# Performance work log

Measured on AMD Instinct MI355X. Metric: run time of the kernel, lower is better.

## Reference

```python
import jax, jax.numpy as jnp
import numpy as np

N = 1024       # nodes
D1 = 64        # hidden_dim_1
D2 = 64        # hidden_dim_2
E = 16384      # edges
P = 8192       # query pairs
MAXX = 100     # max node label -> Embedding(MAXX+1, D1)
EPS = 1e-5     # LayerNorm eps (no affine)


def _ln(t):
    m = jnp.mean(t, axis=-1, keepdims=True)
    v = jnp.mean((t - m) ** 2, axis=-1, keepdims=True)
    return (t - m) / jnp.sqrt(v + EPS)


def setup_inputs() -> dict:
    key = jax.random.key(0)
    ks = jax.random.split(key, 12)
    s = 0.1
    x = jax.random.randint(ks[0], (N,), 0, MAXX + 1)
    ei = jax.random.randint(ks[1], (2, E), 0, N)
    pos = jax.random.randint(ks[2], (P, 2), 0, N)
    emb = jax.random.normal(ks[3], (MAXX + 1, D1)) * s
    sage_Wl = jax.random.normal(ks[4], (2, D1, D1)) * s   # lin_l weight (aggr path, has bias)
    sage_bl = jnp.zeros((2, D1))
    sage_Wr = jax.random.normal(ks[5], (2, D1, D1)) * s   # lin_r weight (root path, no bias)
    h_W = jax.random.normal(ks[6], (D1 + 1, D2)) * s
    h_b = jnp.zeros((D2,))
    g_W = jax.random.normal(ks[7], (D1 + 1 + 2 * D2, D2)) * s
    g_b = jnp.zeros((D2,))
    lin_W = jax.random.normal(ks[8], (D2, 1)) * s
    lin_b = jnp.zeros((1,))
    return {"x": x, "ei": ei, "pos": pos, "emb": emb,
            "sage_Wl": sage_Wl, "sage_bl": sage_bl, "sage_Wr": sage_Wr,
            "h_W": h_W, "h_b": h_b, "g_W": g_W, "g_b": g_b,
            "lin_W": lin_W, "lin_b": lin_b}


def reference(x, ei, pos, emb, sage_Wl, sage_bl, sage_Wr, h_W, h_b, g_W, g_b, lin_W, lin_b):
    n = N
    src, dst = ei[0], ei[1]
    h = emb[x]                                            # (n, D1)
    # SAGEConv x2: mean-aggregate src->dst, lin_l(aggr)+bias + lin_r(root); then LN (no affine, no relu)
    deg = jax.ops.segment_sum(jnp.ones((E,), h.dtype), dst, num_segments=n)
    deg = jnp.maximum(deg, 1.0)[:, None]
    for i in range(2):
        aggr = jax.ops.segment_sum(h[src], dst, num_segments=n) / deg
        h = _ln(aggr @ sage_Wl[i] + sage_bl[i] + h @ sage_Wr[i])
    # pairwise outer product features: (n, n, D1)
    A = h[:, None, :] * h[None, :, :]
    eim = jnp.zeros((n * n,), h.dtype).at[src * n + dst].set(1.0).reshape(n, n, 1)
    A = jnp.concatenate([A, eim], axis=-1)                # (n, n, D1+1)
    # mataggr: B = h_1(A); row/col sums; D = cat(A, vec_p, vec_q); g_1(D)
    B = jax.nn.relu(_ln(A @ h_W + h_b))                   # (n, n, D2)
    vec_p = jnp.sum(B, axis=1, keepdims=True)             # (n, 1, D2)
    vec_q = jnp.sum(B, axis=0, keepdims=True)             # (1, n, D2)
    Dm = jnp.concatenate([A,
                          jnp.broadcast_to(vec_p, (n, n, D2)),
                          jnp.broadcast_to(vec_q, (n, n, D2))], axis=-1)
    G = jax.nn.relu(_ln(Dm @ g_W + g_b))                  # (n, n, D2)
    # symmetrize and gather query pairs
    S = (G * jnp.transpose(G, (1, 0, 2))).reshape(n * n, D2)
    sel = S[pos[:, 0] * n + pos[:, 1]]                    # (P, D2)
    return sel @ lin_W + lin_b                            # (P, 1)
```

## Files before the change

kernel.cpp:

```cpp
#include <hip/hip_runtime.h>
#include <hip/hip_bf16.h>

#define NN 1024
#define DD 64
#define EE 16384
#define PP 8192
#define EPSF 1e-5f
#define SWP (DD + 8)

typedef __hip_bfloat16 bf16;
typedef __attribute__((ext_vector_type(8))) short short8;
typedef __attribute__((ext_vector_type(4))) float f32x4;

static __device__ __forceinline__ float dec1(const void* src, int i, int fl) {
    if (fl) return ((const float*)src)[i];
    return __bfloat162float(((const bf16*)src)[i]);
}
static __device__ __forceinline__ unsigned short f2bf_u(float f) {
    bf16 h = __float2bfloat16(f);
    return *reinterpret_cast<unsigned short*>(&h);
}
static __device__ __forceinline__ float bfu2f(unsigned short u) {
    return __uint_as_float(((unsigned int)u) << 16);
}
static __device__ __forceinline__ int probe_fl(const void* emb) {
    int lane = threadIdx.x & 63;
    unsigned short raw = ((const unsigned short*)emb)[lane];
    float v = __uint_as_float(((unsigned int)raw) << 16);
    return (__ballot(!(fabsf(v) <= 1e3f)) != 0ull) ? 1 : 0;
}

__global__ __launch_bounds__(256) void k_prep(
        const void* __restrict__ emb, const void* __restrict__ sWl,
        const void* __restrict__ sbl, const void* __restrict__ sWr,
        const void* __restrict__ hW, const void* __restrict__ hb,
        const void* __restrict__ gW, const void* __restrict__ gb,
        const void* __restrict__ lW, const void* __restrict__ lb,
        const int* __restrict__ x, const int* __restrict__ ei,
        float* __restrict__ Wlf, float* __restrict__ blf, float* __restrict__ Wrf,
        float* __restrict__ WfT, float* __restrict__ hbw,
        float* __restrict__ gWf, float* __restrict__ linf,
        float* __restrict__ h0,
        unsigned int* __restrict__ eim, unsigned int* __restrict__ eimT,
        int* __restrict__ rowptr, int* __restrict__ csrc) {
    __shared__ int sdeg[NN];
    __shared__ int stmp[256];
    const int b = blockIdx.x, tid = threadIdx.x;
    const int fl = probe_fl(emb);

    if (b < 256) {
        int z = b * 256 + tid;
        if (z < 32768) eim[z] = 0u;
        else           eimT[z - 32768] = 0u;
    }

    if (b < 32) { int i = b * 256 + tid; Wlf[i] = dec1(sWl, i, fl); }
    else if (b == 32) { if (tid < 128) blf[tid] = dec1(sbl, tid, fl); }
    else if (b < 65) { int i = (b - 33) * 256 + tid; Wrf[i] = dec1(sWr, i, fl); }
    else if (b < 82) {
        int i = (b - 65) * 256 + tid;
        if (i < 4096) { int n = i >> 6, k = i & 63; WfT[n * DD + k] = dec1(hW, k * DD + n, fl); }
        else if (i < 4160) hbw[i - 4096] = dec1(hb, i - 4096, fl);
        else if (i < 4224) hbw[64 + (i - 4160)] = dec1(hW, 64 * DD + (i - 4160), fl);
    } else if (b < 131) {
        int i = (b - 82) * 256 + tid;
        if (i < 193 * DD) gWf[i] = dec1(gW, i, fl);
        else if (i < 194 * DD) gWf[i] = dec1(gb, i - 193 * DD, fl);
    } else if (b == 131) {
        if (tid < DD) linf[tid] = dec1(lW, tid, fl);
        else if (tid == DD) linf[DD] = dec1(lb, 0, fl);
    } else if (b < 388) {
        int i = (b - 132) * 256 + tid;
        int node = i >> 6, f = i & 63;
        h0[i] = dec1(emb, x[node] * DD + f, fl);
    } else if (b == 388) {
        for (int i = tid; i < NN; i += 256) sdeg[i] = 0;
        __syncthreads();
        for (int base = 0; base < EE; base += 2048) {
            int d8[8];
#pragma unroll
            for (int u = 0; u < 8; ++u) d8[u] = ei[EE + base + u * 256 + tid];
#pragma unroll
            for (int u = 0; u < 8; ++u) atomicAdd(&sdeg[d8[u]], 1);
        }
        __syncthreads();
        int base4 = tid * 4;
        int v[4]; int s = 0;
#pragma unroll
        for (int u = 0; u < 4; ++u) { v[u] = sdeg[base4 + u]; s += v[u]; }
        stmp[tid] = s;
        __syncthreads();
        for (int off = 1; off < 256; off <<= 1) {
            int a = (tid >= off) ? stmp[tid - off] : 0;
            __syncthreads();
            stmp[tid] += a;
            __syncthreads();
        }
        int run = stmp[tid] - s;
#pragma unroll
        for (int u = 0; u < 4; ++u) {
            rowptr[base4 + u] = run;
            sdeg[base4 + u] = run;
            run += v[u];
        }
        if (tid == 255) rowptr[NN] = run;
        __syncthreads();
        for (int base = 0; base < EE; base += 2048) {
            int d8[8], s8[8];
#pragma unroll
            for (int u = 0; u < 8; ++u) {
                d8[u] = ei[EE + base + u * 256 + tid];
                s8[u] = ei[base + u * 256 + tid];
            }
#pragma unroll
            for (int u = 0; u < 8; ++u) {
                int c = atomicAdd(&sdeg[d8[u]], 1);
                csrc[c] = s8[u];
            }
        }
    }
}

static __device__ __forceinline__ void sage_body(
        char* smem, int node, int lane, int wave,
        const int* __restrict__ rowptr, const int* __restrict__ csrc,
        const float* __restrict__ hin,
        const float* __restrict__ Wl, const float* __restrict__ bl,
        const float* __restrict__ Wr,
        float* __restrict__ hout, unsigned short* __restrict__ hbf) {
    float* sa = (float*)smem + wave * 2 * DD;
    float* sh = sa + DD;
    int r0 = rowptr[node], r1 = rowptr[node + 1];
    float s = 0.f;
    for (int r = r0; r < r1; ++r) s += hin[csrc[r] * DD + lane];
    sa[lane] = s / (float)max(r1 - r0, 1);
    sh[lane] = hin[node * DD + lane];
    float o = bl[lane];
    for (int k = 0; k < DD; ++k)
        o += sa[k] * Wl[k * DD + lane] + sh[k] * Wr[k * DD + lane];
    float m = o;
    for (int off = 32; off; off >>= 1) m += __shfl_xor(m, off);
    m *= (1.f / DD);
    float d0 = o - m;
    float v = d0 * d0;
    for (int off = 32; off; off >>= 1) v += __shfl_xor(v, off);
    v *= (1.f / DD);
    float r = d0 * rsqrtf(v + EPSF);
    hout[node * DD + lane] = r;
    if (hbf) hbf[node * DD + lane] = f2bf_u(r);
}

__global__ __launch_bounds__(256) void k_sage0(
        const int* __restrict__ ei,
        const int* __restrict__ rowptr, const int* __restrict__ csrc,
        const float* __restrict__ h0,
        const float* __restrict__ Wlf, const float* __restrict__ blf,
        const float* __restrict__ Wrf,
        float* __restrict__ h1,
        unsigned int* __restrict__ eim, unsigned int* __restrict__ eimT) {
    __shared__ __align__(16) char smem[4 * 2 * DD * 4];
    const int b = blockIdx.x, tid = threadIdx.x;
    const int lane = tid & 63, wave = tid >> 6;
    if (tid < 64) {
        int e = b * 64 + tid;
        int s = ei[e], d = ei[EE + e];
        unsigned int idx = (unsigned int)(s * NN + d);
        atomicOr(&eim[idx >> 5], 1u << (idx & 31));
        unsigned int idxT = (unsigned int)(d * NN + s);
        atomicOr(&eimT[idxT >> 5], 1u << (idxT & 31));
    }
    sage_body(smem, b * 4 + wave, lane, wave, rowptr, csrc, h0, Wlf, blf, Wrf,
              h1, (unsigned short*)nullptr);
}

__global__ __launch_bounds__(256) void k_sage1(
        const int* __restrict__ rowptr, const int* __restrict__ csrc,
        const float* __restrict__ h1,
        const float* __restrict__ Wlf, const float* __restrict__ blf,
        const float* __restrict__ Wrf,
        float* __restrict__ h2, unsigned short* __restrict__ hbf) {
    __shared__ __align__(16) char smem[4 * 2 * DD * 4];
    const int b = blockIdx.x, tid = threadIdx.x;
    const int lane = tid & 63, wave = tid >> 6;
    sage_body(smem, b * 4 + wave, lane, wave, rowptr, csrc, h1,
              Wlf + DD * DD, blf + DD, Wrf + DD * DD, h2, hbf);
}

__global__ __launch_bounds__(256) void k_bstage(
        const float* __restrict__ h2, const unsigned short* __restrict__ hbf,
        const float* __restrict__ WfT, const float* __restrict__ hbw,
        const unsigned int* __restrict__ eim, const unsigned int* __restrict__ eimT,
        const float* __restrict__ gWf,
        float* __restrict__ ppb, float* __restrict__ qqb) {
    __shared__ __align__(16) unsigned short sW[DD * SWP];
    __shared__ __align__(16) float red[4 * 128];
    const int b = blockIdx.x, tid = threadIdx.x;
    const int lane = tid & 63, wave = tid >> 6;
    const int l15 = lane & 15, quad = lane >> 4;

    {
        int m = tid >> 2;
        int k0 = (tid & 3) * 16;
        const float* hi = h2 + b * DD;
        const float* wr = WfT + m * DD;
        unsigned short tmp[16];
#pragma unroll
        for (int u = 0; u < 16; ++u) tmp[u] = f2bf_u(hi[k0 + u] * wr[k0 + u]);
        *(short8*)(sW + m * SWP + k0) = *(short8*)tmp;
        *(short8*)(sW + m * SWP + k0 + 8) = *(short8*)(tmp + 8);
    }
    __syncthreads();

    short8 Af[4][2];
#pragma unroll
    for (int mt = 0; mt < 4; ++mt)
#pragma unroll
        for (int kt = 0; kt < 2; ++kt)
            Af[mt][kt] = *(const short8*)(sW + (mt * 16 + l15) * SWP + kt * 32 + quad * 8);

    float hb0[4][4], hww[4][4];
#pragma unroll
    for (int mt = 0; mt < 4; ++mt) {
        f32x4 a = *(const f32x4*)(hbw + mt * 16 + quad * 4);
        f32x4 wv = *(const f32x4*)(hbw + 64 + mt * 16 + quad * 4);
#pragma unroll
        for (int r = 0; r < 4; ++r) { hb0[mt][r] = a[r]; hww[mt][r] = wv[r]; }
    }

    float accf[4][4], accb[4][4];
#pragma unroll
    for (int mt = 0; mt < 4; ++mt)
#pragma unroll
        for (int r = 0; r < 4; ++r) { accf[mt][r] = 0.f; accb[mt][r] = 0.f; }

    int g = wave;
    short8 B0 = *(const short8*)(hbf + (g * 16 + l15) * DD + quad * 8);
    short8 B1 = *(const short8*)(hbf + (g * 16 + l15) * DD + 32 + quad * 8);

    for (int it = 0; it < 16; ++it, g += 4) {
        short8 cB0 = B0, cB1 = B1;
        if (it < 15) {
            int gn = g + 4;
            B0 = *(const short8*)(hbf + (gn * 16 + l15) * DD + quad * 8);
            B1 = *(const short8*)(hbf + (gn * 16 + l15) * DD + 32 + quad * 8);
        }
        unsigned int base = (unsigned int)(b * NN + g * 16);
        unsigned int sf = (eim[base >> 5] >> (base & 31)) & 0xFFFFu;
        unsigned int sb = (eimT[base >> 5] >> (base & 31)) & 0xFFFFu;

        f32x4 C[4];
#pragma unroll
        for (int mt = 0; mt < 4; ++mt)
            C[mt] = (f32x4){hb0[mt][0], hb0[mt][1], hb0[mt][2], hb0[mt][3]};
#pragma unroll
        for (int mt = 0; mt < 4; ++mt)
            C[mt] = __builtin_amdgcn_mfma_f32_16x16x32_bf16(Af[mt][0], cB0, C[mt], 0, 0, 0);
#pragma unroll
        for (int mt = 0; mt < 4; ++mt)
            C[mt] = __builtin_amdgcn_mfma_f32_16x16x32_bf16(Af[mt][1], cB1, C[mt], 0, 0, 0);

        float ef = (float)((sf >> l15) & 1u);
        float s1 = 0.f, s2 = 0.f;
#pragma unroll
        for (int mt = 0; mt < 4; ++mt)
#pragma unroll
            for (int r = 0; r < 4; ++r) {
                float v = C[mt][r] + ef * hww[mt][r];
                C[mt][r] = v;
                s1 += v;
                s2 += v * v;
            }
        s1 += __shfl_xor(s1, 16); s1 += __shfl_xor(s1, 32);
        s2 += __shfl_xor(s2, 16); s2 += __shfl_xor(s2, 32);
        float mean = s1 * (1.f / DD);
        float var = fmaxf(s2 * (1.f / DD) - mean * mean, 0.f);
        float rs = rsqrtf(var + EPSF);
        float mrs = mean * rs;

        if (sf == sb) {
#pragma unroll
            for (int mt = 0; mt < 4; ++mt)
#pragma unroll
                for (int r = 0; r < 4; ++r) {
                    float u = fmaxf(C[mt][r] * rs - mrs, 0.f);
                    accf[mt][r] += u;
                    accb[mt][r] += u;
                }
        } else {
#pragma unroll
            for (int mt = 0; mt < 4; ++mt)
#pragma unroll
                for (int r = 0; r < 4; ++r)
                    accf[mt][r] += fmaxf(C[mt][r] * rs - mrs, 0.f);
            float de = (float)((sb >> l15) & 1u) - ef;
            float t1 = 0.f, t2 = 0.f;
#pragma unroll
            for (int mt = 0; mt < 4; ++mt)
#pragma unroll
                for (int r = 0; r < 4; ++r) {
                    float v = C[mt][r] + de * hww[mt][r];
                    C[mt][r] = v;
                    t1 += v;
                    t2 += v * v;
                }
            t1 += __shfl_xor(t1, 16); t1 += __shfl_xor(t1, 32);
            t2 += __shfl_xor(t2, 16); t2 += __shfl_xor(t2, 32);
            float mean2 = t1 * (1.f / DD);
            float var2 = fmaxf(t2 * (1.f / DD) - mean2 * mean2, 0.f);
            float rs2 = rsqrtf(var2 + EPSF);
            float mrs2 = mean2 * rs2;
#pragma unroll
            for (int mt = 0; mt < 4; ++mt)
#pragma unroll
                for (int r = 0; r < 4; ++r)
                    accb[mt][r] += fmaxf(C[mt][r] * rs2 - mrs2, 0.f);
        }
    }

#pragma unroll
    for (int step = 1; step < 16; step <<= 1)
#pragma unroll
        for (int mt = 0; mt < 4; ++mt)
#pragma unroll
            for (int r = 0; r < 4; ++r) {
                accf[mt][r] += __shfl_xor(accf[mt][r], step);
                accb[mt][r] += __shfl_xor(accb[mt][r], step);
            }
    if (l15 == 0) {
#pragma unroll
        for (int mt = 0; mt < 4; ++mt)
#pragma unroll
            for (int r = 0; r < 4; ++r) {
                int m = mt * 16 + quad * 4 + r;
                red[wave * 128 + m] = accf[mt][r];
                red[wave * 128 + DD + m] = accb[mt][r];
            }
    }
    __syncthreads();
    if (tid < 128) {
        float sum = red[tid] + red[128 + tid] + red[256 + tid] + red[384 + tid];
        red[tid] = sum;
    }
    __syncthreads();
    if (wave < 2) {
        const float* sv = red + wave * DD;
        int row0 = wave ? 129 : 65;
        float o = 0.f;
        for (int k = 0; k < DD; ++k) o += sv[k] * gWf[(row0 + k) * DD + lane];
        (wave ? qqb : ppb)[b * DD + lane] = o;
    }
}

__global__ __launch_bounds__(256) void k_final(
        const void* __restrict__ emb,
        const int* __restrict__ pos, const unsigned short* __restrict__ hbf,
        const float* __restrict__ gWf, const unsigned int* __restrict__ eim,
        const float* __restrict__ ppb, const float* __restrict__ qqb,
        const float* __restrict__ linf, void* __restrict__ outv) {
    __shared__ __align__(16) unsigned short sgW[DD * SWP];
    const int b = blockIdx.x, tid = threadIdx.x;
    const int lane = tid & 63, wave = tid >> 6;
    const int l15 = lane & 15, quad = lane >> 4;
    const int fl = probe_fl(emb);

    {
        int m = tid >> 2;
        int k0 = (tid & 3) * 16;
        unsigned short tmp[16];
#pragma unroll
        for (int u = 0; u < 16; ++u) tmp[u] = f2bf_u(gWf[(k0 + u) * DD + m]);
        *(short8*)(sgW + m * SWP + k0) = *(short8*)tmp;
        *(short8*)(sgW + m * SWP + k0 + 8) = *(short8*)(tmp + 8);
    }

    int pp_ = b * 64 + wave * 16 + l15;
    int a = pos[2 * pp_], bb = pos[2 * pp_ + 1];
    short8 ha0 = *(const short8*)(hbf + a * DD + quad * 8);
    short8 hb0v = *(const short8*)(hbf + bb * DD + quad * 8);
    short8 ha1 = *(const short8*)(hbf + a * DD + 32 + quad * 8);
    short8 hb1v = *(const short8*)(hbf + bb * DD + 32 + quad * 8);
    short8 B0, B1;
#pragma unroll
    for (int j = 0; j < 8; ++j) {
        B0[j] = (short)f2bf_u(bfu2f((unsigned short)ha0[j]) * bfu2f((unsigned short)hb0v[j]));
        B1[j] = (short)f2bf_u(bfu2f((unsigned short)ha1[j]) * bfu2f((unsigned short)hb1v[j]));
    }
    __syncthreads();

    f32x4 C[4];
#pragma unroll
    for (int mt = 0; mt < 4; ++mt) C[mt] = (f32x4){0.f, 0.f, 0.f, 0.f};
#pragma unroll
    for (int mt = 0; mt < 4; ++mt) {
        short8 A0 = *(const short8*)(sgW + (mt * 16 + l15) * SWP + quad * 8);
        C[mt] = __builtin_amdgcn_mfma_f32_16x16x32_bf16(A0, B0, C[mt], 0, 0, 0);
    }
#pragma unroll
    for (int mt = 0; mt < 4; ++mt) {
        short8 A1 = *(const short8*)(sgW + (mt * 16 + l15) * SWP + 32 + quad * 8);
        C[mt] = __builtin_amdgcn_mfma_f32_16x16x32_bf16(A1, B1, C[mt], 0, 0, 0);
    }

    unsigned int iab = (unsigned int)(a * NN + bb), iba = (unsigned int)(bb * NN + a);
    float eab = (float)((eim[iab >> 5] >> (iab & 31)) & 1u);
    float eba = (float)((eim[iba >> 5] >> (iba & 31)) & 1u);

    float u1[4][4], u2[4][4];
    float s1 = 0.f, s12 = 0.f, s2 = 0.f, s22 = 0.f;
#pragma unroll
    for (int mt = 0; mt < 4; ++mt) {
        int m0 = mt * 16 + quad * 4;
        f32x4 w64v = *(const f32x4*)(gWf + 64 * DD + m0);
        f32x4 gbv  = *(const f32x4*)(gWf + 193 * DD + m0);
        f32x4 ppa  = *(const f32x4*)(ppb + a * DD + m0);
        f32x4 qqb_ = *(const f32x4*)(qqb + bb * DD + m0);
        f32x4 ppb_ = *(const f32x4*)(ppb + bb * DD + m0);
        f32x4 qqa  = *(const f32x4*)(qqb + a * DD + m0);
#pragma unroll
        for (int r = 0; r < 4; ++r) {
            float v1 = C[mt][r] + eab * w64v[r] + ppa[r] + qqb_[r] + gbv[r];
            float v2 = C[mt][r] + eba * w64v[r] + ppb_[r] + qqa[r] + gbv[r];
            u1[mt][r] = v1; u2[mt][r] = v2;
            s1 += v1; s12 += v1 * v1;
            s2 += v2; s22 += v2 * v2;
        }
    }
    s1 += __shfl_xor(s1, 16);  s1 += __shfl_xor(s1, 32);
    s12 += __shfl_xor(s12, 16); s12 += __shfl_xor(s12, 32);
    s2 += __shfl_xor(s2, 16);  s2 += __shfl_xor(s2, 32);
    s22 += __shfl_xor(s22, 16); s22 += __shfl_xor(s22, 32);
    float mean1 = s1 * (1.f / DD);
    float rs1 = rsqrtf(fmaxf(s12 * (1.f / DD) - mean1 * mean1, 0.f) + EPSF);
    float mrs1 = mean1 * rs1;
    float mean2 = s2 * (1.f / DD);
    float rs2 = rsqrtf(fmaxf(s22 * (1.f / DD) - mean2 * mean2, 0.f) + EPSF);
    float mrs2 = mean2 * rs2;

    float r = 0.f;
#pragma unroll
    for (int mt = 0; mt < 4; ++mt) {
        f32x4 lw = *(const f32x4*)(linf + mt * 16 + quad * 4);
#pragma unroll
        for (int rr = 0; rr < 4; ++rr) {
            float g1 = fmaxf(u1[mt][rr] * rs1 - mrs1, 0.f);
            float g2 = fmaxf(u2[mt][rr] * rs2 - mrs2, 0.f);
            r += g1 * g2 * lw[rr];
        }
    }
    r += __shfl_xor(r, 16); r += __shfl_xor(r, 32);
    if (quad == 0) {
        float res = r + linf[DD];
        if (fl) ((float*)outv)[pp_] = res;
        else    ((bf16*)outv)[pp_] = __float2bfloat16(res);
    }
}

extern "C" void kernel_launch(void* const* d_in, const int* in_sizes, int n_in,
                              void* d_out, int out_size, void* d_ws, size_t ws_size,
                              hipStream_t stream) {
    const int* x   = (const int*)d_in[0];
    const int* ei  = (const int*)d_in[1];
    const int* pos = (const int*)d_in[2];
    const void* emb = d_in[3];

    char* w = (char*)d_ws;
    auto alloc = [&](size_t bytes) {
        void* q = (void*)w;
        w += (bytes + 255) & ~(size_t)255;
        return q;
    };
    unsigned int* eim  = (unsigned int*)alloc(NN * NN / 8);
    unsigned int* eimT = (unsigned int*)alloc(NN * NN / 8);
    float* h0   = (float*)alloc(NN * DD * 4);
    float* h1   = (float*)alloc(NN * DD * 4);
    float* h2   = (float*)alloc(NN * DD * 4);
    unsigned short* hbf = (unsigned short*)alloc(NN * DD * 2);
    float* Wlf  = (float*)alloc(2 * DD * DD * 4);
    float* blf  = (float*)alloc(2 * DD * 4);
    float* Wrf  = (float*)alloc(2 * DD * DD * 4);
    float* WfT  = (float*)alloc(DD * DD * 4);
    float* hbw  = (float*)alloc(128 * 4);
    float* gWf  = (float*)alloc(194 * DD * 4);
    float* linf = (float*)alloc(65 * 4);
    float* ppb  = (float*)alloc(NN * DD * 4);
    float* qqb  = (float*)alloc(NN * DD * 4);
    int* rowptr = (int*)alloc((NN + 1) * 4);
    int* csrc   = (int*)alloc(EE * 4);

    k_prep<<<389, 256, 0, stream>>>(emb, d_in[4], d_in[5], d_in[6], d_in[7], d_in[8],
                                    d_in[9], d_in[10], d_in[11], d_in[12],
                                    x, ei, Wlf, blf, Wrf, WfT, hbw, gWf, linf,
                                    h0, eim, eimT, rowptr, csrc);
    k_sage0<<<256, 256, 0, stream>>>(ei, rowptr, csrc, h0, Wlf, blf, Wrf, h1, eim, eimT);
    k_sage1<<<256, 256, 0, stream>>>(rowptr, csrc, h1, Wlf, blf, Wrf, h2, hbf);
    k_bstage<<<NN, 256, 0, stream>>>(h2, hbf, WfT, hbw, eim, eimT, gWf, ppb, qqb);
    k_final<<<PP / 64, 256, 0, stream>>>(emb, pos, hbf, gWf, eim, ppb, qqb, linf, d_out);
}
```

Measured before the change: 161.6 us.

## Fuse prep into SAGE kernels by scanning all edges per block

Removes the separate prep kernel (CSR build, weight decode, embedding gather, adjacency bitmap clearing). Each SAGE block now scans the full edge list and keeps only the edges whose destination is one of its 4 nodes. It accumulates the neighbour features and degrees with shared-memory atomics, builds its own rows of the adjacency bitmaps, and reads the raw weights directly. This drops one launch and the serial single-block CSR construction. In exchange, each of the 256 blocks reads all 16K edges, so every SAGE layer does redundant edge-list traffic.

After: 174.1 us. +7.7%, slower.

```diff
diff --git a/kernel.cpp b/kernel.cpp
--- a/kernel.cpp
+++ b/kernel.cpp
@@ -30,114 +30,8 @@
     return (__ballot(!(fabsf(v) <= 1e3f)) != 0ull) ? 1 : 0;
 }
 
-__global__ __launch_bounds__(256) void k_prep(
-        const void* __restrict__ emb, const void* __restrict__ sWl,
-        const void* __restrict__ sbl, const void* __restrict__ sWr,
-        const void* __restrict__ hW, const void* __restrict__ hb,
-        const void* __restrict__ gW, const void* __restrict__ gb,
-        const void* __restrict__ lW, const void* __restrict__ lb,
-        const int* __restrict__ x, const int* __restrict__ ei,
-        float* __restrict__ Wlf, float* __restrict__ blf, float* __restrict__ Wrf,
-        float* __restrict__ WfT, float* __restrict__ hbw,
-        float* __restrict__ gWf, float* __restrict__ linf,
-        float* __restrict__ h0,
-        unsigned int* __restrict__ eim, unsigned int* __restrict__ eimT,
-        int* __restrict__ rowptr, int* __restrict__ csrc) {
-    __shared__ int sdeg[NN];
-    __shared__ int stmp[256];
-    const int b = blockIdx.x, tid = threadIdx.x;
-    const int fl = probe_fl(emb);
-
-    if (b < 256) {
-        int z = b * 256 + tid;
-        if (z < 32768) eim[z] = 0u;
-        else           eimT[z - 32768] = 0u;
-    }
-
-    if (b < 32) { int i = b * 256 + tid; Wlf[i] = dec1(sWl, i, fl); }
-    else if (b == 32) { if (tid < 128) blf[tid] = dec1(sbl, tid, fl); }
-    else if (b < 65) { int i = (b - 33) * 256 + tid; Wrf[i] = dec1(sWr, i, fl); }
-    else if (b < 82) {
-        int i = (b - 65) * 256 + tid;
-        if (i < 4096) { int n = i >> 6, k = i & 63; WfT[n * DD + k] = dec1(hW, k * DD + n, fl); }
-        else if (i < 4160) hbw[i - 4096] = dec1(hb, i - 4096, fl);
-        else if (i < 4224) hbw[64 + (i - 4160)] = dec1(hW, 64 * DD + (i - 4160), fl);
-    } else if (b < 131) {
-        int i = (b - 82) * 256 + tid;
-        if (i < 193 * DD) gWf[i] = dec1(gW, i, fl);
-        else if (i < 194 * DD) gWf[i] = dec1(gb, i - 193 * DD, fl);
-    } else if (b == 131) {
-        if (tid < DD) linf[tid] = dec1(lW, tid, fl);
-        else if (tid == DD) linf[DD] = dec1(lb, 0, fl);
-    } else if (b < 388) {
-        int i = (b - 132) * 256 + tid;
-        int node = i >> 6, f = i & 63;
-        h0[i] = dec1(emb, x[node] * DD + f, fl);
-    } else if (b == 388) {
-        for (int i = tid; i < NN; i += 256) sdeg[i] = 0;
-        __syncthreads();
-        for (int base = 0; base < EE; base += 2048) {
-            int d8[8];
-#pragma unroll
-            for (int u = 0; u < 8; ++u) d8[u] = ei[EE + base + u * 256 + tid];
-#pragma unroll
-            for (int u = 0; u < 8; ++u) atomicAdd(&sdeg[d8[u]], 1);
-        }
-        __syncthreads();
-        int base4 = tid * 4;
-        int v[4]; int s = 0;
-#pragma unroll
-        for (int u = 0; u < 4; ++u) { v[u] = sdeg[base4 + u]; s += v[u]; }
-        stmp[tid] = s;
-        __syncthreads();
-        for (int off = 1; off < 256; off <<= 1) {
-            int a = (tid >= off) ? stmp[tid - off] : 0;
-            __syncthreads();
-            stmp[tid] += a;
-            __syncthreads();
-        }
-        int run = stmp[tid] - s;
-#pragma unroll
-        for (int u = 0; u < 4; ++u) {
-            rowptr[base4 + u] = run;
-            sdeg[base4 + u] = run;
-            run += v[u];
-        }
-        if (tid == 255) rowptr[NN] = run;
-        __syncthreads();
-        for (int base = 0; base < EE; base += 2048) {
-            int d8[8], s8[8];
-#pragma unroll
-            for (int u = 0; u < 8; ++u) {
-                d8[u] = ei[EE + base + u * 256 + tid];
-                s8[u] = ei[base + u * 256 + tid];
-            }
-#pragma unroll
-            for (int u = 0; u < 8; ++u) {
-                int c = atomicAdd(&sdeg[d8[u]], 1);
-                csrc[c] = s8[u];
-            }
-        }
-    }
-}
-
-static __device__ __forceinline__ void sage_body(
-        char* smem, int node, int lane, int wave,
-        const int* __restrict__ rowptr, const int* __restrict__ csrc,
-        const float* __restrict__ hin,
-        const float* __restrict__ Wl, const float* __restrict__ bl,
-        const float* __restrict__ Wr,
+static __device__ __forceinline__ void ln_write(float o, int node, int lane,
         float* __restrict__ hout, unsigned short* __restrict__ hbf) {
-    float* sa = (float*)smem + wave * 2 * DD;
-    float* sh = sa + DD;
-    int r0 = rowptr[node], r1 = rowptr[node + 1];
-    float s = 0.f;
-    for (int r = r0; r < r1; ++r) s += hin[csrc[r] * DD + lane];
-    sa[lane] = s / (float)max(r1 - r0, 1);
-    sh[lane] = hin[node * DD + lane];
-    float o = bl[lane];
-    for (int k = 0; k < DD; ++k)
-        o += sa[k] * Wl[k * DD + lane] + sh[k] * Wr[k * DD + lane];
     float m = o;
     for (int off = 32; off; off >>= 1) m += __shfl_xor(m, off);
     m *= (1.f / DD);
@@ -151,39 +45,161 @@
 }
 
 __global__ __launch_bounds__(256) void k_sage0(
-        const int* __restrict__ ei,
-        const int* __restrict__ rowptr, const int* __restrict__ csrc,
-        const float* __restrict__ h0,
-        const float* __restrict__ Wlf, const float* __restrict__ blf,
-        const float* __restrict__ Wrf,
+        const void* __restrict__ emb, const int* __restrict__ x, const int* __restrict__ ei,
+        const void* __restrict__ sWl, const void* __restrict__ sbl, const void* __restrict__ sWr,
+        const void* __restrict__ hW, const void* __restrict__ hb,
+        const void* __restrict__ gW, const void* __restrict__ gb,
+        const void* __restrict__ lW, const void* __restrict__ lb,
         float* __restrict__ h1,
-        unsigned int* __restrict__ eim, unsigned int* __restrict__ eimT) {
-    __shared__ __align__(16) char smem[4 * 2 * DD * 4];
+        unsigned int* __restrict__ eim, unsigned int* __restrict__ eimT,
+        float* __restrict__ WfT, float* __restrict__ hbw,
+        float* __restrict__ gWf, float* __restrict__ linf) {
     const int b = blockIdx.x, tid = threadIdx.x;
+    const int fl = probe_fl(emb);
+
+    if (b >= 256) {
+        int bp = b - 256;
+        if (bp < 17) {
+            int i = bp * 256 + tid;
+            if (i < 4096) { int n = i >> 6, k = i & 63; WfT[n * DD + k] = dec1(hW, k * DD + n, fl); }
+            else if (i < 4160) hbw[i - 4096] = dec1(hb, i - 4096, fl);
+            else if (i < 4224) hbw[64 + (i - 4160)] = dec1(hW, 64 * DD + (i - 4160), fl);
+        } else if (bp < 66) {
+            int i = (bp - 17) * 256 + tid;
+            if (i < 193 * DD) gWf[i] = dec1(gW, i, fl);
+            else if (i < 194 * DD) gWf[i] = dec1(gb, i - 193 * DD, fl);
+        } else {
+            if (tid < DD) linf[tid] = dec1(lW, tid, fl);
+            else if (tid == DD) linf[DD] = dec1(lb, 0, fl);
+        }
+        return;
+    }
+
+    __shared__ float sa[4 * DD];
+    __shared__ float shs[4 * DD];
+    __shared__ unsigned int bmS[128], bmD[128];
+    __shared__ int degl[4];
+    __shared__ int xl[NN];
     const int lane = tid & 63, wave = tid >> 6;
-    if (tid < 64) {
-        int e = b * 64 + tid;
-        int s = ei[e], d = ei[EE + e];
-        unsigned int idx = (unsigned int)(s * NN + d);
-        atomicOr(&eim[idx >> 5], 1u << (idx & 31));
-        unsigned int idxT = (unsigned int)(d * NN + s);
-        atomicOr(&eimT[idxT >> 5], 1u << (idxT & 31));
-    }
-    sage_body(smem, b * 4 + wave, lane, wave, rowptr, csrc, h0, Wlf, blf, Wrf,
-              h1, (unsigned short*)nullptr);
+    const int n0 = b * 4;
+
+    sa[tid] = 0.f;
+    if (tid < 128) { bmS[tid] = 0u; bmD[tid] = 0u; }
+    if (tid < 4) degl[tid] = 0;
+    for (int i = tid; i < NN; i += 256) xl[i] = x[i];
+    __syncthreads();
+
+    for (int base = 0; base < EE; base += 2048) {
+        int s8[8], d8[8];
+#pragma unroll
+        for (int u = 0; u < 8; ++u) {
+            s8[u] = ei[base + u * 256 + tid];
+            d8[u] = ei[EE + base + u * 256 + tid];
+        }
+#pragma unroll
+        for (int u = 0; u < 8; ++u) {
+            int s = s8[u], d = d8[u];
+            if ((unsigned)(s - n0) < 4u)
+                atomicOr(&bmS[(s - n0) * 32 + (d >> 5)], 1u << (d & 31));
+            bool md = ((unsigned)(d - n0) < 4u);
+            if (md) {
+                atomicAdd(&degl[d - n0], 1);
+                atomicOr(&bmD[(d - n0) * 32 + (s >> 5)], 1u << (s & 31));
+            }
+            unsigned long long mask = __ballot(md);
+            while (mask) {
+                int l = __ffsll(mask) - 1; mask &= mask - 1;
+                int sv = __shfl(s, l);
+                int dl_ = __shfl(d, l) - n0;
+                float hv = dec1(emb, xl[sv] * DD + lane, fl);
+                atomicAdd(&sa[dl_ * DD + lane], hv);
+            }
+        }
+    }
+    shs[wave * DD + lane] = dec1(emb, xl[n0 + wave] * DD + lane, fl);
+    __syncthreads();
+
+    if (tid < 128) {
+        eim[n0 * 32 + tid] = bmS[tid];
+        eimT[n0 * 32 + tid] = bmD[tid];
+    }
+
+    float inv = 1.f / (float)max(degl[wave], 1);
+    float o = dec1(sbl, lane, fl);
+    const float* sav = sa + wave * DD;
+    const float* shv = shs + wave * DD;
+    if (fl) {
+        const float* wl = (const float*)sWl;
+        const float* wr = (const float*)sWr;
+        for (int k = 0; k < DD; ++k)
+            o += (sav[k] * inv) * wl[k * DD + lane] + shv[k] * wr[k * DD + lane];
+    } else {
+        const unsigned short* wl = (const unsigned short*)sWl;
+        const unsigned short* wr = (const unsigned short*)sWr;
+        for (int k = 0; k < DD; ++k)
+            o += (sav[k] * inv) * bfu2f(wl[k * DD + lane]) + shv[k] * bfu2f(wr[k * DD + lane]);
+    }
+    ln_write(o, n0 + wave, lane, h1, (unsigned short*)nullptr);
 }
 
 __global__ __launch_bounds__(256) void k_sage1(
-        const int* __restrict__ rowptr, const int* __restrict__ csrc,
+        const void* __restrict__ emb, const int* __restrict__ ei,
+        const void* __restrict__ sWl, const void* __restrict__ sbl, const void* __restrict__ sWr,
         const float* __restrict__ h1,
-        const float* __restrict__ Wlf, const float* __restrict__ blf,
-        const float* __restrict__ Wrf,
         float* __restrict__ h2, unsigned short* __restrict__ hbf) {
-    __shared__ __align__(16) char smem[4 * 2 * DD * 4];
     const int b = blockIdx.x, tid = threadIdx.x;
+    const int fl = probe_fl(emb);
+    __shared__ float sa[4 * DD];
+    __shared__ float shs[4 * DD];
+    __shared__ int degl[4];
     const int lane = tid & 63, wave = tid >> 6;
-    sage_body(smem, b * 4 + wave, lane, wave, rowptr, csrc, h1,
-              Wlf + DD * DD, blf + DD, Wrf + DD * DD, h2, hbf);
+    const int n0 = b * 4;
+
+    sa[tid] = 0.f;
+    if (tid < 4) degl[tid] = 0;
+    __syncthreads();
+
+    for (int base = 0; base < EE; base += 2048) {
+        int s8[8], d8[8];
+#pragma unroll
+        for (int u = 0; u < 8; ++u) {
+            s8[u] = ei[base + u * 256 + tid];
+            d8[u] = ei[EE + base + u * 256 + tid];
+        }
+#pragma unroll
+        for (int u = 0; u < 8; ++u) {
+            int s = s8[u], d = d8[u];
+            bool md = ((unsigned)(d - n0) < 4u);
+            if (md) atomicAdd(&degl[d - n0], 1);
+            unsigned long long mask = __ballot(md);
+            while (mask) {
+                int l = __ffsll(mask) - 1; mask &= mask - 1;
+                int sv = __shfl(s, l);
+                int dl_ = __shfl(d, l) - n0;
+                float hv = h1[sv * DD + lane];
+                atomicAdd(&sa[dl_ * DD + lane], hv);
+            }
+        }
+    }
+    shs[wave * DD + lane] = h1[(n0 + wave) * DD + lane];
+    __syncthreads();
+
+    float inv = 1.f / (float)max(degl[wave], 1);
+    float o = dec1(sbl, DD + lane, fl);
+    const float* sav = sa + wave * DD;
+    const float* shv = shs + wave * DD;
+    if (fl) {
+        const float* wl = (const float*)sWl + DD * DD;
+        const float* wr = (const float*)sWr + DD * DD;
+        for (int k = 0; k < DD; ++k)
+            o += (sav[k] * inv) * wl[k * DD + lane] + shv[k] * wr[k * DD + lane];
+    } else {
+        const unsigned short* wl = (const unsigned short*)sWl + DD * DD;
+        const unsigned short* wr = (const unsigned short*)sWr + DD * DD;
+        for (int k = 0; k < DD; ++k)
+            o += (sav[k] * inv) * bfu2f(wl[k * DD + lane]) + shv[k] * bfu2f(wr[k * DD + lane]);
+    }
+    ln_write(o, n0 + wave, lane, h2, hbf);
 }
 
 __global__ __launch_bounds__(256) void k_bstage(
@@ -471,28 +487,21 @@
     };
     unsigned int* eim  = (unsigned int*)alloc(NN * NN / 8);
     unsigned int* eimT = (unsigned int*)alloc(NN * NN / 8);
-    float* h0   = (float*)alloc(NN * DD * 4);
     float* h1   = (float*)alloc(NN * DD * 4);
     float* h2   = (float*)alloc(NN * DD * 4);
     unsigned short* hbf = (unsigned short*)alloc(NN * DD * 2);
-    float* Wlf  = (float*)alloc(2 * DD * DD * 4);
-    float* blf  = (float*)alloc(2 * DD * 4);
-    float* Wrf  = (float*)alloc(2 * DD * DD * 4);
     float* WfT  = (float*)alloc(DD * DD * 4);
     float* hbw  = (float*)alloc(128 * 4);
     float* gWf  = (float*)alloc(194 * DD * 4);
     float* linf = (float*)alloc(65 * 4);
     float* ppb  = (float*)alloc(NN * DD * 4);
     float* qqb  = (float*)alloc(NN * DD * 4);
-    int* rowptr = (int*)alloc((NN + 1) * 4);
-    int* csrc   = (int*)alloc(EE * 4);
-
-    k_prep<<<389, 256, 0, stream>>>(emb, d_in[4], d_in[5], d_in[6], d_in[7], d_in[8],
-                                    d_in[9], d_in[10], d_in[11], d_in[12],
-                                    x, ei, Wlf, blf, Wrf, WfT, hbw, gWf, linf,
-                                    h0, eim, eimT, rowptr, csrc);
-    k_sage0<<<256, 256, 0, stream>>>(ei, rowptr, csrc, h0, Wlf, blf, Wrf, h1, eim, eimT);
-    k_sage1<<<256, 256, 0, stream>>>(rowptr, csrc, h1, Wlf, blf, Wrf, h2, hbf);
+
+    k_sage0<<<323, 256, 0, stream>>>(emb, x, ei, d_in[4], d_in[5], d_in[6],
+                                     d_in[7], d_in[8], d_in[9], d_in[10],
+                                     d_in[11], d_in[12],
+                                     h1, eim, eimT, WfT, hbw, gWf, linf);
+    k_sage1<<<256, 256, 0, stream>>>(emb, ei, d_in[4], d_in[5], d_in[6], h1, h2, hbf);
     k_bstage<<<NN, 256, 0, stream>>>(h2, hbf, WfT, hbw, eim, eimT, gWf, ppb, qqb);
     k_final<<<PP / 64, 256, 0, stream>>>(emb, pos, hbf, gWf, eim, ppb, qqb, linf, d_out);
 }
```

## Split bstage rows across two blocks, pair MFMA tiles, move projection to new kernel

Applied to the files above, without the earlier changes.

Each row's column sweep in k_bstage is now split across two blocks, giving 2048 blocks instead of 1024. Each wave processes two 16-column tiles per iteration, so the eim/eimT mask words are loaded once per 32 columns. The partial row and column sums go to new scratch buffers. A new k_ppqq2 kernel adds the two halves and applies the gW projection. The aim is more parallelism and more independent MFMA work to hide latency, at the cost of an extra launch and extra global traffic.

Result: slower. 168.7 us (+4.4%).

```diff
diff --git a/kernel.cpp b/kernel.cpp
--- a/kernel.cpp
+++ b/kernel.cpp
@@ -186,22 +186,84 @@
               Wlf + DD * DD, blf + DD, Wrf + DD * DD, h2, hbf);
 }
 
+static __device__ __forceinline__ void tile_ln(
+        f32x4* C, unsigned int sf, unsigned int sb, int l15,
+        const float hww[4][4], float accf[4][4], float accb[4][4]) {
+    float ef = (float)((sf >> l15) & 1u);
+    float s1 = 0.f, s2 = 0.f;
+#pragma unroll
+    for (int mt = 0; mt < 4; ++mt)
+#pragma unroll
+        for (int r = 0; r < 4; ++r) {
+            float v = C[mt][r] + ef * hww[mt][r];
+            C[mt][r] = v;
+            s1 += v;
+            s2 += v * v;
+        }
+    s1 += __shfl_xor(s1, 16); s1 += __shfl_xor(s1, 32);
+    s2 += __shfl_xor(s2, 16); s2 += __shfl_xor(s2, 32);
+    float mean = s1 * (1.f / DD);
+    float var = fmaxf(s2 * (1.f / DD) - mean * mean, 0.f);
+    float rs = rsqrtf(var + EPSF);
+    float mrs = mean * rs;
+
+    if (sf == sb) {
+#pragma unroll
+        for (int mt = 0; mt < 4; ++mt)
+#pragma unroll
+            for (int r = 0; r < 4; ++r) {
+                float u = fmaxf(C[mt][r] * rs - mrs, 0.f);
+                accf[mt][r] += u;
+                accb[mt][r] += u;
+            }
+    } else {
+#pragma unroll
+        for (int mt = 0; mt < 4; ++mt)
+#pragma unroll
+            for (int r = 0; r < 4; ++r)
+                accf[mt][r] += fmaxf(C[mt][r] * rs - mrs, 0.f);
+        float de = (float)((sb >> l15) & 1u) - ef;
+        float t1 = 0.f, t2 = 0.f;
+#pragma unroll
+        for (int mt = 0; mt < 4; ++mt)
+#pragma unroll
+            for (int r = 0; r < 4; ++r) {
+                float v = C[mt][r] + de * hww[mt][r];
+                C[mt][r] = v;
+                t1 += v;
+                t2 += v * v;
+            }
+        t1 += __shfl_xor(t1, 16); t1 += __shfl_xor(t1, 32);
+        t2 += __shfl_xor(t2, 16); t2 += __shfl_xor(t2, 32);
+        float mean2 = t1 * (1.f / DD);
+        float var2 = fmaxf(t2 * (1.f / DD) - mean2 * mean2, 0.f);
+        float rs2 = rsqrtf(var2 + EPSF);
+        float mrs2 = mean2 * rs2;
+#pragma unroll
+        for (int mt = 0; mt < 4; ++mt)
+#pragma unroll
+            for (int r = 0; r < 4; ++r)
+                accb[mt][r] += fmaxf(C[mt][r] * rs2 - mrs2, 0.f);
+    }
+}
+
 __global__ __launch_bounds__(256) void k_bstage(
         const float* __restrict__ h2, const unsigned short* __restrict__ hbf,
         const float* __restrict__ WfT, const float* __restrict__ hbw,
         const unsigned int* __restrict__ eim, const unsigned int* __restrict__ eimT,
-        const float* __restrict__ gWf,
-        float* __restrict__ ppb, float* __restrict__ qqb) {
+        float* __restrict__ vpp, float* __restrict__ vqp) {
     __shared__ __align__(16) unsigned short sW[DD * SWP];
     __shared__ __align__(16) float red[4 * 128];
-    const int b = blockIdx.x, tid = threadIdx.x;
+    const int bid = blockIdx.x;
+    const int fix = bid >> 1, half = bid & 1;
+    const int tid = threadIdx.x;
     const int lane = tid & 63, wave = tid >> 6;
     const int l15 = lane & 15, quad = lane >> 4;
 
     {
         int m = tid >> 2;
         int k0 = (tid & 3) * 16;
-        const float* hi = h2 + b * DD;
+        const float* hi = h2 + fix * DD;
         const float* wr = WfT + m * DD;
         unsigned short tmp[16];
 #pragma unroll
@@ -233,88 +295,47 @@
 #pragma unroll
         for (int r = 0; r < 4; ++r) { accf[mt][r] = 0.f; accb[mt][r] = 0.f; }
 
-    int g = wave;
-    short8 B0 = *(const short8*)(hbf + (g * 16 + l15) * DD + quad * 8);
-    short8 B1 = *(const short8*)(hbf + (g * 16 + l15) * DD + 32 + quad * 8);
-
-    for (int it = 0; it < 16; ++it, g += 4) {
-        short8 cB0 = B0, cB1 = B1;
-        if (it < 15) {
-            int gn = g + 4;
-            B0 = *(const short8*)(hbf + (gn * 16 + l15) * DD + quad * 8);
-            B1 = *(const short8*)(hbf + (gn * 16 + l15) * DD + 32 + quad * 8);
-        }
-        unsigned int base = (unsigned int)(b * NN + g * 16);
-        unsigned int sf = (eim[base >> 5] >> (base & 31)) & 0xFFFFu;
-        unsigned int sb = (eimT[base >> 5] >> (base & 31)) & 0xFFFFu;
-
-        f32x4 C[4];
-#pragma unroll
-        for (int mt = 0; mt < 4; ++mt)
-            C[mt] = (f32x4){hb0[mt][0], hb0[mt][1], hb0[mt][2], hb0[mt][3]};
-#pragma unroll
-        for (int mt = 0; mt < 4; ++mt)
-            C[mt] = __builtin_amdgcn_mfma_f32_16x16x32_bf16(Af[mt][0], cB0, C[mt], 0, 0, 0);
-#pragma unroll
-        for (int mt = 0; mt < 4; ++mt)
-            C[mt] = __builtin_amdgcn_mfma_f32_16x16x32_bf16(Af[mt][1], cB1, C[mt], 0, 0, 0);
-
-        float ef = (float)((sf >> l15) & 1u);
-        float s1 = 0.f, s2 = 0.f;
-#pragma unroll
-        for (int mt = 0; mt < 4; ++mt)
-#pragma unroll
-            for (int r = 0; r < 4; ++r) {
-                float v = C[mt][r] + ef * hww[mt][r];
-                C[mt][r] = v;
-                s1 += v;
-                s2 += v * v;
-            }
-        s1 += __shfl_xor(s1, 16); s1 += __shfl_xor(s1, 32);
-        s2 += __shfl_xor(s2, 16); s2 += __shfl_xor(s2, 32);
-        float mean = s1 * (1.f / DD);
-        float var = fmaxf(s2 * (1.f / DD) - mean * mean, 0.f);
-        float rs = rsqrtf(var + EPSF);
-        float mrs = mean * rs;
-
-        if (sf == sb) {
-#pragma unroll
-            for (int mt = 0; mt < 4; ++mt)
-#pragma unroll
-                for (int r = 0; r < 4; ++r) {
-                    float u = fmaxf(C[mt][r] * rs - mrs, 0.f);
-                    accf[mt][r] += u;
-                    accb[mt][r] += u;
-                }
-        } else {
-#pragma unroll
-            for (int mt = 0; mt < 4; ++mt)
-#pragma unroll
-                for (int r = 0; r < 4; ++r)
-                    accf[mt][r] += fmaxf(C[mt][r] * rs - mrs, 0.f);
-            float de = (float)((sb >> l15) & 1u) - ef;
-            float t1 = 0.f, t2 = 0.f;
-#pragma unroll
-            for (int mt = 0; mt < 4; ++mt)
-#pragma unroll
-                for (int r = 0; r < 4; ++r) {
-                    float v = C[mt][r] + de * hww[mt][r];
-                    C[mt][r] = v;
-                    t1 += v;
-                    t2 += v * v;
-                }
-            t1 += __shfl_xor(t1, 16); t1 += __shfl_xor(t1, 32);
-            t2 += __shfl_xor(t2, 16); t2 += __shfl_xor(t2, 32);
-            float mean2 = t1 * (1.f / DD);
-            float var2 = fmaxf(t2 * (1.f / DD) - mean2 * mean2, 0.f);
-            float rs2 = rsqrtf(var2 + EPSF);
-            float mrs2 = mean2 * rs2;
-#pragma unroll
-            for (int mt = 0; mt < 4; ++mt)
-#pragma unroll
-                for (int r = 0; r < 4; ++r)
-                    accb[mt][r] += fmaxf(C[mt][r] * rs2 - mrs2, 0.f);
-        }
+    const int g0 = half * 32 + wave * 8;
+    short8 B0a = *(const short8*)(hbf + (g0 * 16 + l15) * DD + quad * 8);
+    short8 B1a = *(const short8*)(hbf + (g0 * 16 + l15) * DD + 32 + quad * 8);
+    short8 B0b = *(const short8*)(hbf + ((g0 + 1) * 16 + l15) * DD + quad * 8);
+    short8 B1b = *(const short8*)(hbf + ((g0 + 1) * 16 + l15) * DD + 32 + quad * 8);
+
+    for (int it = 0; it < 4; ++it) {
+        int g = g0 + it * 2;
+        short8 cB0a = B0a, cB1a = B1a, cB0b = B0b, cB1b = B1b;
+        if (it < 3) {
+            int gn = g + 2;
+            B0a = *(const short8*)(hbf + (gn * 16 + l15) * DD + quad * 8);
+            B1a = *(const short8*)(hbf + (gn * 16 + l15) * DD + 32 + quad * 8);
+            B0b = *(const short8*)(hbf + ((gn + 1) * 16 + l15) * DD + quad * 8);
+            B1b = *(const short8*)(hbf + ((gn + 1) * 16 + l15) * DD + 32 + quad * 8);
+        }
+        unsigned int widx = (unsigned int)(fix * NN + g * 16) >> 5;
+        unsigned int wf = eim[widx];
+        unsigned int wb = eimT[widx];
+
+        f32x4 Ca[4], Cb[4];
+#pragma unroll
+        for (int mt = 0; mt < 4; ++mt) {
+            Ca[mt] = (f32x4){hb0[mt][0], hb0[mt][1], hb0[mt][2], hb0[mt][3]};
+            Cb[mt] = Ca[mt];
+        }
+#pragma unroll
+        for (int mt = 0; mt < 4; ++mt)
+            Ca[mt] = __builtin_amdgcn_mfma_f32_16x16x32_bf16(Af[mt][0], cB0a, Ca[mt], 0, 0, 0);
+#pragma unroll
+        for (int mt = 0; mt < 4; ++mt)
+            Ca[mt] = __builtin_amdgcn_mfma_f32_16x16x32_bf16(Af[mt][1], cB1a, Ca[mt], 0, 0, 0);
+#pragma unroll
+        for (int mt = 0; mt < 4; ++mt)
+            Cb[mt] = __builtin_amdgcn_mfma_f32_16x16x32_bf16(Af[mt][0], cB0b, Cb[mt], 0, 0, 0);
+#pragma unroll
+        for (int mt = 0; mt < 4; ++mt)
+            Cb[mt] = __builtin_amdgcn_mfma_f32_16x16x32_bf16(Af[mt][1], cB1b, Cb[mt], 0, 0, 0);
+
+        tile_ln(Ca, wf & 0xFFFFu, wb & 0xFFFFu, l15, hww, accf, accb);
+        tile_ln(Cb, wf >> 16, wb >> 16, l15, hww, accf, accb);
     }
 
 #pragma unroll
@@ -337,18 +358,27 @@
             }
     }
     __syncthreads();
-    if (tid < 128) {
+    if (tid < 2 * DD) {
         float sum = red[tid] + red[128 + tid] + red[256 + tid] + red[384 + tid];
-        red[tid] = sum;
-    }
+        if (tid < DD) vpp[(half * NN + fix) * DD + tid] = sum;
+        else          vqp[(half * NN + fix) * DD + (tid - DD)] = sum;
+    }
+}
+
+__global__ void k_ppqq2(const float* __restrict__ vpp, const float* __restrict__ vqp,
+                        const float* __restrict__ gWf,
+                        float* __restrict__ ppb, float* __restrict__ qqb) {
+    int b = blockIdx.x;
+    int f = threadIdx.x;
+    int i = b & 1023, which = b >> 10;
+    const float* part = which ? vqp : vpp;
+    int row0 = which ? 129 : 65;
+    __shared__ float sv[DD];
+    sv[f] = part[i * DD + f] + part[(NN + i) * DD + f];
     __syncthreads();
-    if (wave < 2) {
-        const float* sv = red + wave * DD;
-        int row0 = wave ? 129 : 65;
-        float o = 0.f;
-        for (int k = 0; k < DD; ++k) o += sv[k] * gWf[(row0 + k) * DD + lane];
-        (wave ? qqb : ppb)[b * DD + lane] = o;
-    }
+    float o = 0.f;
+    for (int k = 0; k < DD; ++k) o += sv[k] * gWf[(row0 + k) * DD + f];
+    (which ? qqb : ppb)[i * DD + f] = o;
 }
 
 __global__ __launch_bounds__(256) void k_final(
@@ -482,6 +512,8 @@
     float* hbw  = (float*)alloc(128 * 4);
     float* gWf  = (float*)alloc(194 * DD * 4);
     float* linf = (float*)alloc(65 * 4);
+    float* vpp  = (float*)alloc(2 * NN * DD * 4);
+    float* vqp  = (float*)alloc(2 * NN * DD * 4);
     float* ppb  = (float*)alloc(NN * DD * 4);
     float* qqb  = (float*)alloc(NN * DD * 4);
     int* rowptr = (int*)alloc((NN + 1) * 4);
@@ -493,6 +525,7 @@
                                     h0, eim, eimT, rowptr, csrc);
     k_sage0<<<256, 256, 0, stream>>>(ei, rowptr, csrc, h0, Wlf, blf, Wrf, h1, eim, eimT);
     k_sage1<<<256, 256, 0, stream>>>(rowptr, csrc, h1, Wlf, blf, Wrf, h2, hbf);
-    k_bstage<<<NN, 256, 0, stream>>>(h2, hbf, WfT, hbw, eim, eimT, gWf, ppb, qqb);
+    k_bstage<<<2 * NN, 256, 0, stream>>>(h2, hbf, WfT, hbw, eim, eimT, vpp, vqp);
+    k_ppqq2<<<2 * NN, DD, 0, stream>>>(vpp, vqp, gWf, ppb, qqb);
     k_final<<<PP / 64, 256, 0, stream>>>(emb, pos, hbf, gWf, eim, ppb, qqb, linf, d_out);
 }
```
